# Kernel tuning notes

Measured on AMD Instinct MI355X. Metric: run time of the kernel, lower is better.

## Reference

```python
import jax, jax.numpy as jnp
import numpy as np

B, N, DIM = 4, 8192, 512
HEADS, DIM_HEAD, M, ITERS = 8, 64, 256, 6
KERNEL = 33


def moore_penrose_pinv(x, iters=ITERS):
    # x: [..., m, m]
    abs_x = jnp.abs(x)
    col = abs_x.sum(axis=-1)
    row = abs_x.sum(axis=-2)
    z = jnp.swapaxes(x, -1, -2) / (jnp.max(col) * jnp.max(row))
    I = jnp.eye(x.shape[-1], dtype=x.dtype)
    for _ in range(iters):
        xz = x @ z
        z = 0.25 * z @ (13.0 * I - xz @ (15.0 * I - xz @ (7.0 * I - xz)))
    return z


def setup_inputs() -> dict:
    key = jax.random.key(0)
    k1, k2, k3, k4 = jax.random.split(key, 4)
    x = jax.random.normal(k1, (B, N, DIM), dtype=jnp.float32)
    w_qkv = jax.random.normal(k2, (DIM, 3 * HEADS * DIM_HEAD), dtype=jnp.float32) * 0.02
    w_out = jax.random.normal(k3, (HEADS * DIM_HEAD, DIM), dtype=jnp.float32) * 0.02
    b_out = jnp.zeros((DIM,), dtype=jnp.float32)
    w_conv = jax.random.normal(k4, (HEADS, 1, KERNEL, 1), dtype=jnp.float32) * 0.02
    return {"x": x, "w_qkv": w_qkv, "w_out": w_out, "b_out": b_out, "w_conv": w_conv}


def reference(x, w_qkv, w_out, b_out, w_conv):
    b, n, _ = x.shape
    h, d, m = HEADS, DIM_HEAD, M
    scale = d ** -0.5
    l = n // m  # n is a multiple of m here (padding path is a no-op)

    qkv = x @ w_qkv  # [b, n, 3*h*d]
    q, k, v = jnp.split(qkv, 3, axis=-1)
    to_heads = lambda t: jnp.transpose(t.reshape(b, n, h, d), (0, 2, 1, 3))  # [b,h,n,d]
    q, k, v = to_heads(q), to_heads(k), to_heads(v)

    q = q * scale
    # landmarks: mean over contiguous blocks of length l
    q_land = q.reshape(b, h, m, l, d).sum(axis=3) / l  # [b,h,m,d]
    k_land = k.reshape(b, h, m, l, d).sum(axis=3) / l

    attn1 = jax.nn.softmax(jnp.einsum('bhid,bhjd->bhij', q, k_land), axis=-1)       # [b,h,n,m]
    attn2 = jax.nn.softmax(jnp.einsum('bhid,bhjd->bhij', q_land, k_land), axis=-1)  # [b,h,m,m]
    attn3 = jax.nn.softmax(jnp.einsum('bhid,bhjd->bhij', q_land, k), axis=-1)       # [b,h,m,n]

    attn2_pinv = moore_penrose_pinv(attn2, ITERS)
    out = attn1 @ (attn2_pinv @ (attn3 @ v))  # [b,h,n,d]

    # depthwise residual conv over the sequence axis (kernel (33,1), groups=heads)
    pad = KERNEL // 2
    res = jax.lax.conv_general_dilated(
        v, w_conv, window_strides=(1, 1), padding=((pad, pad), (0, 0)),
        dimension_numbers=('NCHW', 'OIHW', 'NCHW'), feature_group_count=h)
    out = out + res

    out = jnp.transpose(out, (0, 2, 1, 3)).reshape(b, n, h * d)
    out = out @ w_out + b_out
    return out
```

## Files before the change

kernel.cpp:

```cpp
#include <hip/hip_runtime.h>
#include <cstdint>
#include <cstddef>

#define BQ 4
#define NSEQ 8192
#define DIMC 512
#define NH 8
#define DH 64
#define NM 256
#define NITER 6
#define KW 33
#define BHN (BQ*NH)
#define NSLICE 8

typedef unsigned short bf16u;
typedef __attribute__((ext_vector_type(8))) short short8;
typedef __attribute__((ext_vector_type(4))) float f32x4;
#define MFMA16(a,b,c) __builtin_amdgcn_mfma_f32_16x16x32_bf16(a,b,c,0,0,0)

__device__ inline float b2f(bf16u u) { return __uint_as_float(((unsigned int)u) << 16); }
__device__ inline bf16u f2b(float f) {
  unsigned int u = __float_as_uint(f);
  unsigned int r = (u + 0x7fffu + ((u >> 16) & 1u)) >> 16;
  return (bf16u)r;
}
__device__ inline void splt(float v, unsigned short& h, unsigned short& l) {
  unsigned u = __float_as_uint(v);
  h = (unsigned short)(u >> 16);
  float hf = __uint_as_float(u & 0xffff0000u);
  l = (unsigned short)(__float_as_uint(v - hf) >> 16);
}

__global__ __launch_bounds__(256) void k_fill(float* out, int n, float v) {
  int i = blockIdx.x * 256 + threadIdx.x;
  if (i < n) out[i] = v;
}

__global__ __launch_bounds__(256) void c_f2b(const float* __restrict__ src, bf16u* __restrict__ dst, int n8) {
  int i = blockIdx.x*256 + threadIdx.x;
  if (i < n8) {
    const float4* s = (const float4*)(src + (size_t)i*8);
    float4 a = s[0], b = s[1];
    ushort4 lo, hi;
    lo.x=f2b(a.x); lo.y=f2b(a.y); lo.z=f2b(a.z); lo.w=f2b(a.w);
    hi.x=f2b(b.x); hi.y=f2b(b.y); hi.z=f2b(b.z); hi.w=f2b(b.w);
    ushort4* d = (ushort4*)(dst + (size_t)i*8);
    d[0] = lo; d[1] = hi;
  }
}

__global__ __launch_bounds__(256) void c_transb(const float* __restrict__ w, bf16u* __restrict__ wT, int R, int C) {
  int i = blockIdx.x*256 + threadIdx.x;
  if (i < R*C) {
    int r = i / C, c = i - r*C;
    wT[(size_t)c*R + r] = f2b(w[i]);
  }
}

template<int MODE>
__global__ __launch_bounds__(256) void k_mgemm(
    const bf16u* __restrict__ A, const bf16u* __restrict__ Bt, int K, int nb,
    bf16u* __restrict__ oq, bf16u* __restrict__ ok, bf16u* __restrict__ ovT,
    const float* __restrict__ bias, float* __restrict__ oC) {
  __shared__ short As[128][72];
  __shared__ short Bs[128][72];
  const int id = blockIdx.x;
  const int rid = (id & 7) * ((int)gridDim.x >> 3) + (id >> 3);
  const int m0 = (rid / nb) * 128, n0 = (rid % nb) * 128;
  const int t = threadIdx.x;
  const int wid = t>>6, l = t&63, lm = l&15, lg = l>>4;
  const int wr = (wid>>1)*64, wc = (wid&1)*64;
  f32x4 acc[4][4];
  #pragma unroll
  for (int i=0;i<4;++i)
    #pragma unroll
    for (int j=0;j<4;++j) acc[i][j] = (f32x4){0,0,0,0};
  for (int k0=0; k0<K; k0+=64) {
    #pragma unroll
    for (int i=0;i<4;++i) {
      int c = t + i*256;
      int row = c>>3, kc = (c&7)<<3;
      *(uint4*)&As[row][kc] = *(const uint4*)(A  + (size_t)(m0+row)*K + k0+kc);
      *(uint4*)&Bs[row][kc] = *(const uint4*)(Bt + (size_t)(n0+row)*K + k0+kc);
    }
    __syncthreads();
    #pragma unroll
    for (int ks=0;ks<2;++ks) {
      short8 af[4], bfr[4];
      #pragma unroll
      for (int i=0;i<4;++i) {
        af[i]  = *(const short8*)&As[wr+i*16+lm][ks*32+lg*8];
        bfr[i] = *(const short8*)&Bs[wc+i*16+lm][ks*32+lg*8];
      }
      #pragma unroll
      for (int i=0;i<4;++i)
        #pragma unroll
        for (int j=0;j<4;++j)
          acc[i][j] = MFMA16(af[i], bfr[j], acc[i][j]);
    }
    __syncthreads();
  }
  if (MODE==0) {
    #pragma unroll
    for (int mt=0;mt<4;++mt) {
      int grb = m0 + wr + mt*16 + lg*4;
      int b_ = grb>>13, nrow = grb & (NSEQ-1);
      #pragma unroll
      for (int nt=0;nt<4;++nt) {
        int gc = n0 + wc + nt*16 + lm;
        int which = gc>>9, h_ = (gc>>6)&7, d = gc&63;
        if (which==2) {
          ushort4 pk;
          pk.x=f2b(acc[mt][nt][0]); pk.y=f2b(acc[mt][nt][1]);
          pk.z=f2b(acc[mt][nt][2]); pk.w=f2b(acc[mt][nt][3]);
          *(ushort4*)(ovT + (((size_t)b_*NH+h_)*DH + d)*NSEQ + nrow) = pk;
        } else {
          bf16u* dst = (which==0) ? oq : ok;
          float mul = (which==0) ? 0.125f : 1.0f;
          #pragma unroll
          for (int r=0;r<4;++r)
            dst[(((size_t)b_*NH+h_)*NSEQ + nrow + r)*DH + d] = f2b(acc[mt][nt][r]*mul);
        }
      }
    }
  } else {
    #pragma unroll
    for (int mt=0;mt<4;++mt)
      #pragma unroll
      for (int r=0;r<4;++r) {
        int gr = m0 + wr + mt*16 + lg*4 + r;
        #pragma unroll
        for (int nt=0;nt<4;++nt) {
          int gc = n0 + wc + nt*16 + lm;
          oC[(size_t)gr*DIMC + gc] = acc[mt][nt][r] + bias[gc];
        }
      }
  }
}

__global__ __launch_bounds__(256) void k_landmarks(
    const bf16u* __restrict__ q, const bf16u* __restrict__ kbuf,
    float* __restrict__ ql, float* __restrict__ klm,
    bf16u* __restrict__ qlb, bf16u* __restrict__ klmb) {
  int gi = blockIdx.x*4 + (threadIdx.x>>6);
  int d = threadIdx.x & 63;
  int bh = gi >> 8, i = gi & 255;
  size_t srcoff = ((size_t)bh*NSEQ + (size_t)i*32)*DH + d;
  float sq = 0, sk = 0;
  #pragma unroll
  for (int j = 0; j < 32; ++j) {
    sq += b2f(q[srcoff + (size_t)j*DH]);
    sk += b2f(kbuf[srcoff + (size_t)j*DH]);
  }
  float mq = sq * (1.0f/32.0f), mk = sk * (1.0f/32.0f);
  ql[(size_t)gi*DH + d]  = mq;  klm[(size_t)gi*DH + d]  = mk;
  qlb[(size_t)gi*DH + d] = f2b(mq); klmb[(size_t)gi*DH + d] = f2b(mk);
}

__global__ __launch_bounds__(256) void k_qlk_exp(
    const float* __restrict__ A, const float* __restrict__ S, float* __restrict__ C, int K) {
  __shared__ short Ah[128][40], Al[128][40], Bh[64][40], Bl[64][40];
  const int bh = blockIdx.y;
  const size_t abase = (size_t)bh*256*K;
  const size_t cbase = (size_t)bh<<16;
  const int m0 = (blockIdx.x & 1)*128, n0 = (blockIdx.x >> 1)*64;
  const int t = threadIdx.x;
  const int wid = t>>6, l = t&63, lm = l&15, lg = l>>4;
  const int wr = (wid&1)*64, wc = (wid>>1)*32;
  f32x4 acc[4][2];
  #pragma unroll
  for (int i=0;i<4;++i) { acc[i][0] = (f32x4){0,0,0,0}; acc[i][1] = (f32x4){0,0,0,0}; }
  for (int k0=0; k0<K; k0+=32) {
    #pragma unroll
    for (int i=0;i<4;++i) {
      int idx = t + i*256;
      int row = idx>>3, kc = (idx&7)<<2;
      float4 v = *(const float4*)(A + abase + (size_t)(m0+row)*K + k0+kc);
      ushort4 hh, ll;
      splt(v.x, hh.x, ll.x); splt(v.y, hh.y, ll.y);
      splt(v.z, hh.z, ll.z); splt(v.w, hh.w, ll.w);
      *(ushort4*)&Ah[row][kc] = hh; *(ushort4*)&Al[row][kc] = ll;
    }
    #pragma unroll
    for (int i=0;i<2;++i) {
      int idx = t + i*256;
      int row = idx>>3, kc = (idx&7)<<2;
      float4 v = *(const float4*)(S + abase + (size_t)(n0+row)*K + k0+kc);
      ushort4 hh, ll;
      splt(v.x, hh.x, ll.x); splt(v.y, hh.y, ll.y);
      splt(v.z, hh.z, ll.z); splt(v.w, hh.w, ll.w);
      *(ushort4*)&Bh[row][kc] = hh; *(ushort4*)&Bl[row][kc] = ll;
    }
    __syncthreads();
    short8 ah[4], al[4], sh[2], sl[2];
    #pragma unroll
    for (int mt=0;mt<4;++mt) {
      ah[mt] = *(const short8*)&Ah[wr+mt*16+lm][lg*8];
      al[mt] = *(const short8*)&Al[wr+mt*16+lm][lg*8];
    }
    #pragma unroll
    for (int nt=0;nt<2;++nt) {
      sh[nt] = *(const short8*)&Bh[wc+nt*16+lm][lg*8];
      sl[nt] = *(const short8*)&Bl[wc+nt*16+lm][lg*8];
    }
    #pragma unroll
    for (int mt=0;mt<4;++mt)
      #pragma unroll
      for (int nt=0;nt<2;++nt) {
        acc[mt][nt] = MFMA16(ah[mt], sh[nt], acc[mt][nt]);
        acc[mt][nt] = MFMA16(ah[mt], sl[nt], acc[mt][nt]);
        acc[mt][nt] = MFMA16(al[mt], sh[nt], acc[mt][nt]);
      }
    __syncthreads();
  }
  #pragma unroll
  for (int mt=0;mt<4;++mt)
    #pragma unroll
    for (int nt=0;nt<2;++nt)
      #pragma unroll
      for (int r=0;r<4;++r) {
        int gr = m0 + wr + mt*16 + lg*4 + r;
        int gc = n0 + wc + nt*16 + lm;
        C[cbase + (size_t)gr*256 + gc] = __expf(acc[mt][nt][r]);
      }
}

__global__ __launch_bounds__(256) void k_rowsm(float* __restrict__ a2) {
  int row = blockIdx.x*4 + (threadIdx.x>>6);
  int l = threadIdx.x & 63;
  float4* p = (float4*)(a2 + (size_t)row*256 + l*4);
  float4 v = *p;
  float s = v.x+v.y+v.z+v.w;
  #pragma unroll
  for (int d=1; d<64; d<<=1) s += __shfl_xor(s, d);
  float inv = 1.0f/s;
  v.x*=inv; v.y*=inv; v.z*=inv; v.w*=inv;
  *p = v;
}

__global__ void k_zero_scal(unsigned* scal) { if (threadIdx.x < 2) scal[threadIdx.x] = 0u; }

__global__ __launch_bounds__(256) void k_pinv_reduce(const float* __restrict__ a2, unsigned* scal) {
  int bh = blockIdx.x, t = threadIdx.x;
  const float* A = a2 + (size_t)bh*NM*NM;
  float rs = 0, cs = 0;
  for (int j = 0; j < NM; ++j) rs += fabsf(A[(size_t)t*NM + j]);
  for (int i = 0; i < NM; ++i) cs += fabsf(A[(size_t)i*NM + t]);
  __shared__ float red[256];
  red[t] = rs; __syncthreads();
  for (int s = 128; s > 0; s >>= 1) { if (t < s) red[t] = fmaxf(red[t], red[t+s]); __syncthreads(); }
  if (t == 0) atomicMax(scal+0, __float_as_uint(red[0]));
  __syncthreads();
  red[t] = cs; __syncthreads();
  for (int s = 128; s > 0; s >>= 1) { if (t < s) red[t] = fmaxf(red[t], red[t+s]); __syncthreads(); }
  if (t == 0) atomicMax(scal+1, __float_as_uint(red[0]));
}

__global__ __launch_bounds__(256) void k_split_init(
    const float* __restrict__ a2, const unsigned* __restrict__ scal,
    bf16u* __restrict__ a2h, bf16u* __restrict__ a2l,
    bf16u* __restrict__ zch, bf16u* __restrict__ zcl) {
  __shared__ bf16u Th[64][72], Tl[64][72];
  const int bh = blockIdx.y;
  const int tx = blockIdx.x & 3, ty = blockIdx.x >> 2;
  const int r0 = ty*64, c0 = tx*64;
  const size_t base = (size_t)bh<<16;
  const int t = threadIdx.x;
  const float rc = 1.0f/(__uint_as_float(scal[0]) * __uint_as_float(scal[1]));
  {
    int rr = t>>2, cc0 = (t&3)*16;
    const float* src = a2 + base + (size_t)(r0+rr)*256 + c0+cc0;
    bf16u hbuf[16], lbuf[16];
    #pragma unroll
    for (int u=0;u<4;++u) {
      float4 v = *(const float4*)(src + u*4);
      float vv[4] = {v.x,v.y,v.z,v.w};
      #pragma unroll
      for (int e=0;e<4;++e) {
        splt(vv[e], hbuf[u*4+e], lbuf[u*4+e]);
        bf16u zh_, zl_;
        splt(vv[e]*rc, zh_, zl_);
        Th[cc0+u*4+e][rr] = zh_;
        Tl[cc0+u*4+e][rr] = zl_;
      }
    }
    bf16u* dh = a2h + base + (size_t)(r0+rr)*256 + c0+cc0;
    bf16u* dl = a2l + base + (size_t)(r0+rr)*256 + c0+cc0;
    #pragma unroll
    for (int u=0;u<4;++u) {
      *(ushort4*)(dh + u*4) = *(ushort4*)&hbuf[u*4];
      *(ushort4*)(dl + u*4) = *(ushort4*)&lbuf[u*4];
    }
  }
  __syncthreads();
  {
    int cc = t>>2, rr0 = (t&3)*16;
    bf16u* dh = zch + base + (size_t)(c0+cc)*256 + r0+rr0;
    bf16u* dl = zcl + base + (size_t)(c0+cc)*256 + r0+rr0;
    #pragma unroll
    for (int u=0;u<4;++u) {
      *(ushort4*)(dh + u*4) = *(ushort4*)&Th[cc][rr0+u*4];
      *(ushort4*)(dl + u*4) = *(ushort4*)&Tl[cc][rr0+u*4];
    }
  }
}

template<int PHASE>
__global__ __launch_bounds__(256) void k_ns(
    const bf16u* __restrict__ Ah, const bf16u* __restrict__ Al,
    const bf16u* __restrict__ A2h, const bf16u* __restrict__ A2l,
    const bf16u* __restrict__ Bh_, const bf16u* __restrict__ Bl_,
    const bf16u* __restrict__ Xh, const bf16u* __restrict__ Xl,
    const bf16u* __restrict__ X2h, const bf16u* __restrict__ X2l,
    bf16u* __restrict__ Oh, bf16u* __restrict__ Ol,
    bf16u* __restrict__ O2h, bf16u* __restrict__ O2l,
    bf16u* __restrict__ Ch, bf16u* __restrict__ Cl,
    const unsigned* __restrict__ scal) {
  __shared__ short AhS[128][36], AlS[128][36], BhS[64][36], BlS[64][36];
  const int z = (gridDim.z == 2) ? blockIdx.z : (PHASE==2 ? 1 : 0);
  const int bh = blockIdx.y;
  const size_t base = (size_t)bh<<16;
  const int m0 = (blockIdx.x & 1)*128, n0 = (blockIdx.x >> 1)*64;
  const int t = threadIdx.x;
  const int wid = t>>6, l = t&63, lm = l&15, lg = l>>4;
  const int wr = (wid&1)*64, wc = (wid>>1)*32;
  const bf16u* pAh = z ? A2h : Ah;
  const bf16u* pAl = z ? A2l : Al;
  f32x4 acc[4][2];
  #pragma unroll
  for (int i=0;i<4;++i) { acc[i][0] = (f32x4){0,0,0,0}; acc[i][1] = (f32x4){0,0,0,0}; }
  for (int k0=0; k0<256; k0+=32) {
    #pragma unroll
    for (int i=0;i<2;++i) {
      int idx = t + i*256;
      int row = idx>>2, ch = (idx&3)<<3;
      *(uint4*)&AhS[row][ch] = *(const uint4*)(pAh + base + (size_t)(m0+row)*256 + k0+ch);
      *(uint4*)&AlS[row][ch] = *(const uint4*)(pAl + base + (size_t)(m0+row)*256 + k0+ch);
    }
    {
      int row = t>>2, ch = (t&3)<<3;
      *(uint4*)&BhS[row][ch] = *(const uint4*)(Bh_ + base + (size_t)(n0+row)*256 + k0+ch);
      *(uint4*)&BlS[row][ch] = *(const uint4*)(Bl_ + base + (size_t)(n0+row)*256 + k0+ch);
    }
    __syncthreads();
    short8 ah[4], al[4], sh[2], sl[2];
    #pragma unroll
    for (int mt=0;mt<4;++mt) {
      ah[mt] = *(const short8*)&AhS[wr+mt*16+lm][lg*8];
      al[mt] = *(const short8*)&AlS[wr+mt*16+lm][lg*8];
    }
    #pragma unroll
    for (int nt=0;nt<2;++nt) {
      sh[nt] = *(const short8*)&BhS[wc+nt*16+lm][lg*8];
      sl[nt] = *(const short8*)&BlS[wc+nt*16+lm][lg*8];
    }
    #pragma unroll
    for (int mt=0;mt<4;++mt)
      #pragma unroll
      for (int nt=0;nt<2;++nt) {
        acc[mt][nt] = MFMA16(ah[mt], sh[nt], acc[mt][nt]);
        acc[mt][nt] = MFMA16(ah[mt], sl[nt], acc[mt][nt]);
        acc[mt][nt] = MFMA16(al[mt], sh[nt], acc[mt][nt]);
      }
    __syncthreads();
  }
  float rc = 1.0f;
  if (PHASE==0) rc = 1.0f/(__uint_as_float(scal[0]) * __uint_as_float(scal[1]));
  #pragma unroll
  for (int mt=0;mt<4;++mt)
    #pragma unroll
    for (int nt=0;nt<2;++nt)
      #pragma unroll
      for (int r=0;r<4;++r) {
        int gr = m0 + wr + mt*16 + lg*4 + r;
        int gc = n0 + wc + nt*16 + lm;
        size_t idx = base + (size_t)gr*256 + gc;
        float a = acc[mt][nt][r];
        bf16u hh, ll;
        if (PHASE==0) {
          splt(a*rc, hh, ll); Oh[idx]=hh; Ol[idx]=ll;
        } else if (PHASE==1) {
          if (z==0) {
            splt(a, hh, ll); Oh[idx]=hh; Ol[idx]=ll;
            float wv = b2f(Xh[idx]) + b2f(Xl[idx]);
            float cb = ((gr==gc)?15.0f:0.0f) - 7.0f*wv + a;
            splt(cb, hh, ll); Ch[idx]=hh; Cl[idx]=ll;
          } else {
            splt(a, hh, ll); O2h[idx]=hh; O2l[idx]=ll;
          }
        } else {
          if (z==0) {
            float xv = b2f(Xh[idx]) + b2f(Xl[idx]);
            splt(3.25f*xv - 0.25f*a, hh, ll); Oh[idx]=hh; Ol[idx]=ll;
          } else {
            float xv = b2f(X2h[idx]) + b2f(X2l[idx]);
            splt(3.25f*xv - 0.25f*a, hh, ll); O2h[idx]=hh; O2l[idx]=ll;
          }
        }
      }
}

template<int MODE>
__global__ __launch_bounds__(256) void k_flash(
    const bf16u* __restrict__ qg, const bf16u* __restrict__ kg,
    const bf16u* __restrict__ vtg, float* __restrict__ fpart, bf16u* __restrict__ outb) {
  constexpr int NCH = (MODE==0) ? 16 : 4;
  const int bh = blockIdx.y;
  const int tile = blockIdx.x;
  const int t = threadIdx.x;
  const int wid = t>>6, l = t&63, lm = l&15, lg = l>>4;
  const size_t NQbase = (MODE==0) ? ((size_t)bh*NM) : ((size_t)bh*NSEQ + (size_t)tile*256);
  const int NJ = (MODE==0) ? NSEQ : NM;
  const int j0base = (MODE==0) ? tile*1024 : 0;

  __shared__ short Ks[64][72];
  __shared__ short Vs[64][72];
  __shared__ short Pt[4][64][72];

  short8 qf[4][2];
  {
    const bf16u* qrow = qg + (NQbase + (size_t)wid*64) * DH;
    #pragma unroll
    for (int mt=0;mt<4;++mt)
      #pragma unroll
      for (int ks=0;ks<2;++ks)
        qf[mt][ks] = *(const short8*)(qrow + (size_t)(mt*16+lm)*DH + ks*32 + lg*8);
  }
  f32x4 oacc[4][4];
  #pragma unroll
  for (int i=0;i<4;++i)
    #pragma unroll
    for (int j=0;j<4;++j) oacc[i][j] = (f32x4){0,0,0,0};
  float rs[4][4];
  #pragma unroll
  for (int i=0;i<4;++i) { rs[i][0]=0; rs[i][1]=0; rs[i][2]=0; rs[i][3]=0; }

  const bf16u* kbh = kg  + (size_t)bh*NJ*DH;
  const bf16u* vbh = vtg + (size_t)bh*DH*NJ;

  for (int ch=0; ch<NCH; ++ch) {
    int j0 = j0base + ch*64;
    #pragma unroll
    for (int i=0;i<2;++i) {
      int c = t + i*256;
      int row = c>>3, kc = (c&7)<<3;
      *(uint4*)&Ks[row][kc] = *(const uint4*)(kbh + (size_t)(j0+row)*DH + kc);
      *(uint4*)&Vs[row][kc] = *(const uint4*)(vbh + (size_t)row*NJ + j0 + kc);
    }
    __syncthreads();
    short8 kf[4][2];
    #pragma unroll
    for (int jt=0;jt<4;++jt)
      #pragma unroll
      for (int ks=0;ks<2;++ks)
        kf[jt][ks] = *(const short8*)&Ks[jt*16+lm][ks*32+lg*8];
    #pragma unroll
    for (int mt=0;mt<4;++mt) {
      #pragma unroll
      for (int jt=0;jt<4;++jt) {
        f32x4 s = (f32x4){0,0,0,0};
        s = MFMA16(qf[mt][0], kf[jt][0], s);
        s = MFMA16(qf[mt][1], kf[jt][1], s);
        #pragma unroll
        for (int r=0;r<4;++r) {
          float p = __expf(s[r]);
          rs[mt][r] += p;
          Pt[wid][mt*16+lg*4+r][jt*16+lm] = f2b(p);
        }
      }
    }
    short8 vf[4][2];
    #pragma unroll
    for (int dt=0;dt<4;++dt)
      #pragma unroll
      for (int jw=0;jw<2;++jw)
        vf[dt][jw] = *(const short8*)&Vs[dt*16+lm][jw*32+lg*8];
    #pragma unroll
    for (int mt=0;mt<4;++mt) {
      short8 pa0 = *(const short8*)&Pt[wid][mt*16+lm][lg*8];
      short8 pa1 = *(const short8*)&Pt[wid][mt*16+lm][32+lg*8];
      #pragma unroll
      for (int dt=0;dt<4;++dt) {
        oacc[mt][dt] = MFMA16(pa0, vf[dt][0], oacc[mt][dt]);
        oacc[mt][dt] = MFMA16(pa1, vf[dt][1], oacc[mt][dt]);
      }
    }
    __syncthreads();
  }
  #pragma unroll
  for (int mt=0;mt<4;++mt)
    #pragma unroll
    for (int r=0;r<4;++r) {
      float v = rs[mt][r];
      v += __shfl_xor(v, 1); v += __shfl_xor(v, 2);
      v += __shfl_xor(v, 4); v += __shfl_xor(v, 8);
      rs[mt][r] = v;
    }
  if (MODE==0) {
    float* fb = fpart + (((size_t)bh*NSLICE + tile)*NM)*65;
    #pragma unroll
    for (int mt=0;mt<4;++mt)
      #pragma unroll
      for (int r=0;r<4;++r) {
        int row = wid*64 + mt*16 + lg*4 + r;
        float* fr = fb + (size_t)row*65;
        #pragma unroll
        for (int dt=0;dt<4;++dt) fr[dt*16+lm] = oacc[mt][dt][r];
        if (lm==0) fr[64] = rs[mt][r];
      }
  } else {
    const int b_ = bh>>3, h_ = bh&7;
    #pragma unroll
    for (int mt=0;mt<4;++mt)
      #pragma unroll
      for (int r=0;r<4;++r) {
        float inv = 1.0f/rs[mt][r];
        int n = tile*256 + wid*64 + mt*16 + lg*4 + r;
        bf16u* orow = outb + ((size_t)b_*NSEQ + n)*DIMC + h_*DH;
        #pragma unroll
        for (int dt=0;dt<4;++dt)
          orow[dt*16+lm] = f2b(oacc[mt][dt][r]*inv);
      }
  }
}

__global__ __launch_bounds__(256) void k_attn3v_combine(
    const float* __restrict__ fpart, float* __restrict__ w1T) {
  int gi = blockIdx.x*4 + (threadIdx.x>>6);
  int d = threadIdx.x & 63;
  int bh = gi >> 8, i = gi & 255;
  float accd = 0, ssum = 0;
  #pragma unroll
  for (int s = 0; s < NSLICE; ++s) {
    const float* fp = fpart + (((size_t)bh*NSLICE + s)*NM + i)*65;
    accd += fp[d];
    ssum += fp[64];
  }
  w1T[((size_t)bh*64 + d)*256 + i] = accd / ssum;
}

__global__ __launch_bounds__(256) void k_w2nat(
    const float* __restrict__ w1T, const bf16u* __restrict__ zh, const bf16u* __restrict__ zl,
    bf16u* __restrict__ w2T) {
  __shared__ short Ah[64][36], Al[64][36], Bh[64][36], Bl[64][36];
  const int bh = blockIdx.y;
  const int n0 = blockIdx.x*64;
  const size_t a0 = (size_t)bh*64*256;
  const size_t s0 = (size_t)bh<<16;
  const int t = threadIdx.x;
  const int wid = t>>6, l = t&63, lm = l&15, lg = l>>4;
  const int wc = wid*16;
  f32x4 acc[4];
  #pragma unroll
  for (int i=0;i<4;++i) acc[i] = (f32x4){0,0,0,0};
  for (int k0=0; k0<256; k0+=32) {
    #pragma unroll
    for (int i=0;i<2;++i) {
      int idx = t + i*256;
      int row = idx>>3, kc = (idx&7)<<2;
      float4 v = *(const float4*)(w1T + a0 + (size_t)row*256 + k0+kc);
      ushort4 hh, ll;
      splt(v.x, hh.x, ll.x); splt(v.y, hh.y, ll.y);
      splt(v.z, hh.z, ll.z); splt(v.w, hh.w, ll.w);
      *(ushort4*)&Ah[row][kc] = hh; *(ushort4*)&Al[row][kc] = ll;
    }
    {
      int row = t>>2, ch = (t&3)<<3;
      *(uint4*)&Bh[row][ch] = *(const uint4*)(zh + s0 + (size_t)(n0+row)*256 + k0+ch);
      *(uint4*)&Bl[row][ch] = *(const uint4*)(zl + s0 + (size_t)(n0+row)*256 + k0+ch);
    }
    __syncthreads();
    short8 sh = *(const short8*)&Bh[wc+lm][lg*8];
    short8 sl = *(const short8*)&Bl[wc+lm][lg*8];
    #pragma unroll
    for (int mt=0;mt<4;++mt) {
      short8 ah = *(const short8*)&Ah[mt*16+lm][lg*8];
      short8 al = *(const short8*)&Al[mt*16+lm][lg*8];
      acc[mt] = MFMA16(ah, sh, acc[mt]);
      acc[mt] = MFMA16(ah, sl, acc[mt]);
      acc[mt] = MFMA16(al, sh, acc[mt]);
    }
    __syncthreads();
  }
  #pragma unroll
  for (int mt=0;mt<4;++mt)
    #pragma unroll
    for (int r=0;r<4;++r) {
      int gm = mt*16 + lg*4 + r;
      w2T[a0 + (size_t)gm*256 + n0 + wc + lm] = f2b(acc[mt][r]);
    }
}

__global__ __launch_bounds__(256) void k_conv_add(
    const bf16u* __restrict__ vt, const float* __restrict__ wc, bf16u* __restrict__ outb) {
  __shared__ short Vs[288][72];
  __shared__ float Wsh[40];
  const int bh = blockIdx.y, n0 = blockIdx.x*256;
  const int b_ = bh>>3, h_ = bh&7;
  const int t = threadIdx.x;
  if (t < KW) Wsh[t] = wc[h_*KW + t];
  const bf16u* vrow = vt + (size_t)bh*DH*NSEQ;
  {
    int d = t&63, seg = t>>6;
    #pragma unroll
    for (int u=0; u<9; ++u) {
      int nl = seg*72 + u*8;
      int gn = n0 - 16 + nl;
      bf16u e8[8];
      if (gn >= 0 && gn + 8 <= NSEQ) {
        *(uint4*)e8 = *(const uint4*)(vrow + (size_t)d*NSEQ + gn);
      } else {
        #pragma unroll
        for (int e=0;e<8;++e) {
          int g = gn + e;
          e8[e] = (g>=0 && g<NSEQ) ? vrow[(size_t)d*NSEQ + g] : (bf16u)0;
        }
      }
      #pragma unroll
      for (int e=0;e<8;++e) Vs[nl+e][d] = e8[e];
    }
  }
  __syncthreads();
  const int d = t&63, q = t>>6;
  #pragma unroll
  for (int c2=0;c2<4;++c2) {
    int nb = q*64 + c2*16;
    float wv[48];
    #pragma unroll
    for (int i=0;i<48;++i) wv[i] = b2f(Vs[nb+i][d]);
    #pragma unroll
    for (int e=0;e<16;++e) {
      float s = 0;
      #pragma unroll
      for (int k=0;k<KW;++k) s = fmaf(wv[e+k], Wsh[k], s);
      size_t oi = ((size_t)b_*NSEQ + n0 + nb + e)*DIMC + h_*DH + d;
      outb[oi] = f2b(b2f(outb[oi]) + s);
    }
  }
}

extern "C" void kernel_launch(void* const* d_in, const int* in_sizes, int n_in,
                              void* d_out, int out_size, void* d_ws, size_t ws_size,
                              hipStream_t stream) {
  (void)in_sizes; (void)n_in;
  const float* x      = (const float*)d_in[0];
  const float* w_qkv  = (const float*)d_in[1];
  const float* w_out  = (const float*)d_in[2];
  const float* b_out  = (const float*)d_in[3];
  const float* w_conv = (const float*)d_in[4];
  float* out = (float*)d_out;

  const size_t QKV_E = (size_t)BHN*NSEQ*DH;
  const size_t LM_E  = (size_t)BHN*NM*DH;
  const size_t MM_E  = (size_t)BHN*NM*NM;
  const size_t PLSZ  = MM_E*2;

  char* p = (char*)d_ws;
  char* nsb   = p;          p += 10*PLSZ;
  bf16u* qb    = (bf16u*)p; p += QKV_E*2;
  bf16u* kb    = (bf16u*)p; p += QKV_E*2;
  bf16u* vT    = (bf16u*)p; p += QKV_E*2;
  bf16u* wqkvT = (bf16u*)p; p += (size_t)DIMC*3*DIMC*2;
  bf16u* woutT = (bf16u*)p; p += (size_t)DIMC*DIMC*2;
  float* ql    = (float*)p; p += LM_E*4;
  float* klm   = (float*)p; p += LM_E*4;
  bf16u* qlb   = (bf16u*)p; p += LM_E*2;
  bf16u* klmb  = (bf16u*)p; p += LM_E*2;
  float* w1T   = (float*)p; p += LM_E*4;
  bf16u* w2T   = (bf16u*)p; p += LM_E*2;
  unsigned* scal = (unsigned*)p; p += 256;
  size_t need = (size_t)(p - (char*)d_ws);

  if (ws_size < need) {
    k_fill<<<(out_size + 255)/256, 256, 0, stream>>>(out, out_size, 12345.0f);
    return;
  }

  bf16u* a2h  = (bf16u*)(nsb + 0*PLSZ);
  bf16u* a2l  = (bf16u*)(nsb + 1*PLSZ);
  bf16u* s1h  = (bf16u*)(nsb + 2*PLSZ);
  bf16u* s1l  = (bf16u*)(nsb + 3*PLSZ);
  bf16u* cmh  = (bf16u*)(nsb + 4*PLSZ);
  bf16u* cml  = (bf16u*)(nsb + 5*PLSZ);
  bf16u* wh   = (bf16u*)(nsb + 6*PLSZ);
  bf16u* wl   = (bf16u*)(nsb + 7*PLSZ);
  bf16u* zch  = (bf16u*)(nsb + 8*PLSZ);
  bf16u* zcl  = (bf16u*)(nsb + 9*PLSZ);
  float* a2f  = (float*)(nsb + 2*PLSZ);
  float* fpart = (float*)nsb;
  bf16u* c1h = a2h; bf16u* c1l = a2l;
  bf16u* xb  = qb;
  xb = (bf16u*)nsb;

  c_f2b<<<(int)(QKV_E/8/256), 256, 0, stream>>>(x, xb, (int)(QKV_E/8));
  c_transb<<<(DIMC*3*DIMC+255)/256, 256, 0, stream>>>(w_qkv, wqkvT, DIMC, 3*DIMC);
  c_transb<<<(DIMC*DIMC+255)/256, 256, 0, stream>>>(w_out, woutT, DIMC, DIMC);
  k_mgemm<0><<<3072, 256, 0, stream>>>(xb, wqkvT, DIMC, 12, qb, kb, vT, nullptr, nullptr);
  k_landmarks<<<(BHN*NM)/4, 256, 0, stream>>>(qb, kb, ql, klm, qlb, klmb);
  k_qlk_exp<<<dim3(8, BHN), 256, 0, stream>>>(ql, klm, a2f, DH);
  k_rowsm<<<BHN*NM/4, 256, 0, stream>>>(a2f);
  k_zero_scal<<<1, 64, 0, stream>>>(scal);
  k_pinv_reduce<<<BHN, 256, 0, stream>>>(a2f, scal);
  k_split_init<<<dim3(16, BHN), 256, 0, stream>>>(a2f, scal, a2h, a2l, zch, zcl);
  k_ns<0><<<dim3(8, BHN, 1), 256, 0, stream>>>(
      a2h,a2l, nullptr,nullptr, a2h,a2l, nullptr,nullptr, nullptr,nullptr,
      wh,wl, nullptr,nullptr, nullptr,nullptr, scal);
  for (int it = 0; it < NITER; ++it) {
    k_ns<1><<<dim3(8, BHN, 2), 256, 0, stream>>>(
        wh,wl, zch,zcl, wh,wl, wh,wl, nullptr,nullptr,
        s1h,s1l, c1h,c1l, cmh,cml, nullptr);
    k_ns<2><<<dim3(8, BHN, (it==NITER-1)?1:2), 256, 0, stream>>>(
        s1h,s1l, c1h,c1l, cmh,cml, wh,wl, zch,zcl,
        wh,wl, zch,zcl, nullptr,nullptr, nullptr);
  }
  k_flash<0><<<dim3(NSLICE, BHN), 256, 0, stream>>>(qlb, kb, vT, fpart, nullptr);
  k_attn3v_combine<<<(BHN*NM)/4, 256, 0, stream>>>(fpart, w1T);
  k_w2nat<<<dim3(4, BHN), 256, 0, stream>>>(w1T, zch, zcl, w2T);
  bf16u* outb = kb;
  k_flash<1><<<dim3(NSEQ/256, BHN), 256, 0, stream>>>(qb, klmb, w2T, nullptr, outb);
  k_conv_add<<<dim3(NSEQ/256, BHN), 256, 0, stream>>>(vT, w_conv, outb);
  k_mgemm<1><<<1024, 256, 0, stream>>>(outb, woutT, DIMC, 4, nullptr, nullptr, nullptr, b_out, out);
}
```

Before: 712.3 us.

## Merge prep conversion kernels, fold scalar zeroing, and double flash split slices

```diff
diff --git a/kernel.cpp b/kernel.cpp
--- a/kernel.cpp
+++ b/kernel.cpp
@@ -11,7 +11,8 @@
 #define NITER 6
 #define KW 33
 #define BHN (BQ*NH)
-#define NSLICE 8
+#define NSLICE 16
+#define JS (NSEQ/NSLICE)
 
 typedef unsigned short bf16u;
 typedef __attribute__((ext_vector_type(8))) short short8;
@@ -36,24 +37,27 @@
   if (i < n) out[i] = v;
 }
 
-__global__ __launch_bounds__(256) void c_f2b(const float* __restrict__ src, bf16u* __restrict__ dst, int n8) {
-  int i = blockIdx.x*256 + threadIdx.x;
-  if (i < n8) {
-    const float4* s = (const float4*)(src + (size_t)i*8);
+__global__ __launch_bounds__(256) void c_prep(
+    const float* __restrict__ x, const float* __restrict__ w_qkv, const float* __restrict__ w_out,
+    bf16u* __restrict__ xb, bf16u* __restrict__ wqkvT, bf16u* __restrict__ woutT) {
+  int id = blockIdx.x;
+  if (id < 8192) {
+    int i = id*256 + threadIdx.x;
+    const float4* s = (const float4*)(x + (size_t)i*8);
     float4 a = s[0], b = s[1];
     ushort4 lo, hi;
     lo.x=f2b(a.x); lo.y=f2b(a.y); lo.z=f2b(a.z); lo.w=f2b(a.w);
     hi.x=f2b(b.x); hi.y=f2b(b.y); hi.z=f2b(b.z); hi.w=f2b(b.w);
-    ushort4* d = (ushort4*)(dst + (size_t)i*8);
+    ushort4* d = (ushort4*)(xb + (size_t)i*8);
     d[0] = lo; d[1] = hi;
-  }
-}
-
-__global__ __launch_bounds__(256) void c_transb(const float* __restrict__ w, bf16u* __restrict__ wT, int R, int C) {
-  int i = blockIdx.x*256 + threadIdx.x;
-  if (i < R*C) {
-    int r = i / C, c = i - r*C;
-    wT[(size_t)c*R + r] = f2b(w[i]);
+  } else if (id < 8192+3072) {
+    int i = (id-8192)*256 + threadIdx.x;
+    int r = i / 1536, c = i - r*1536;
+    wqkvT[(size_t)c*DIMC + r] = f2b(w_qkv[i]);
+  } else {
+    int i = (id-11264)*256 + threadIdx.x;
+    int r = i >> 9, c = i & 511;
+    woutT[(size_t)c*DIMC + r] = f2b(w_out[i]);
   }
 }
 
@@ -225,7 +229,8 @@
       }
 }
 
-__global__ __launch_bounds__(256) void k_rowsm(float* __restrict__ a2) {
+__global__ __launch_bounds__(256) void k_rowsm(float* __restrict__ a2, unsigned* __restrict__ scal) {
+  if (blockIdx.x == 0 && threadIdx.x < 2) scal[threadIdx.x] = 0u;
   int row = blockIdx.x*4 + (threadIdx.x>>6);
   int l = threadIdx.x & 63;
   float4* p = (float4*)(a2 + (size_t)row*256 + l*4);
@@ -237,8 +242,6 @@
   v.x*=inv; v.y*=inv; v.z*=inv; v.w*=inv;
   *p = v;
 }
-
-__global__ void k_zero_scal(unsigned* scal) { if (threadIdx.x < 2) scal[threadIdx.x] = 0u; }
 
 __global__ __launch_bounds__(256) void k_pinv_reduce(const float* __restrict__ a2, unsigned* scal) {
   int bh = blockIdx.x, t = threadIdx.x;
@@ -404,14 +407,14 @@
 __global__ __launch_bounds__(256) void k_flash(
     const bf16u* __restrict__ qg, const bf16u* __restrict__ kg,
     const bf16u* __restrict__ vtg, float* __restrict__ fpart, bf16u* __restrict__ outb) {
-  constexpr int NCH = (MODE==0) ? 16 : 4;
+  constexpr int NCH = (MODE==0) ? (JS/64) : 4;
   const int bh = blockIdx.y;
   const int tile = blockIdx.x;
   const int t = threadIdx.x;
   const int wid = t>>6, l = t&63, lm = l&15, lg = l>>4;
   const size_t NQbase = (MODE==0) ? ((size_t)bh*NM) : ((size_t)bh*NSEQ + (size_t)tile*256);
   const int NJ = (MODE==0) ? NSEQ : NM;
-  const int j0base = (MODE==0) ? tile*1024 : 0;
+  const int j0base = (MODE==0) ? tile*JS : 0;
 
   __shared__ short Ks[64][72];
   __shared__ short Vs[64][72];
@@ -656,7 +659,9 @@
   const size_t PLSZ  = MM_E*2;
 
   char* p = (char*)d_ws;
-  char* nsb   = p;          p += 10*PLSZ;
+  char* nsb   = p;          p += 9*PLSZ;
+  bf16u* zch  = (bf16u*)p;  p += PLSZ;
+  bf16u* zcl  = (bf16u*)p;  p += PLSZ;
   bf16u* qb    = (bf16u*)p; p += QKV_E*2;
   bf16u* kb    = (bf16u*)p; p += QKV_E*2;
   bf16u* vT    = (bf16u*)p; p += QKV_E*2;
@@ -684,22 +689,16 @@
   bf16u* cml  = (bf16u*)(nsb + 5*PLSZ);
   bf16u* wh   = (bf16u*)(nsb + 6*PLSZ);
   bf16u* wl   = (bf16u*)(nsb + 7*PLSZ);
-  bf16u* zch  = (bf16u*)(nsb + 8*PLSZ);
-  bf16u* zcl  = (bf16u*)(nsb + 9*PLSZ);
   float* a2f  = (float*)(nsb + 2*PLSZ);
   float* fpart = (float*)nsb;
   bf16u* c1h = a2h; bf16u* c1l = a2l;
-  bf16u* xb  = qb;
-  xb = (bf16u*)nsb;
-
-  c_f2b<<<(int)(QKV_E/8/256), 256, 0, stream>>>(x, xb, (int)(QKV_E/8));
-  c_transb<<<(DIMC*3*DIMC+255)/256, 256, 0, stream>>>(w_qkv, wqkvT, DIMC, 3*DIMC);
-  c_transb<<<(DIMC*DIMC+255)/256, 256, 0, stream>>>(w_out, woutT, DIMC, DIMC);
+  bf16u* xb  = (bf16u*)nsb;
+
+  c_prep<<<12288, 256, 0, stream>>>(x, w_qkv, w_out, xb, wqkvT, woutT);
   k_mgemm<0><<<3072, 256, 0, stream>>>(xb, wqkvT, DIMC, 12, qb, kb, vT, nullptr, nullptr);
   k_landmarks<<<(BHN*NM)/4, 256, 0, stream>>>(qb, kb, ql, klm, qlb, klmb);
   k_qlk_exp<<<dim3(8, BHN), 256, 0, stream>>>(ql, klm, a2f, DH);
-  k_rowsm<<<BHN*NM/4, 256, 0, stream>>>(a2f);
-  k_zero_scal<<<1, 64, 0, stream>>>(scal);
+  k_rowsm<<<BHN*NM/4, 256, 0, stream>>>(a2f, scal);
   k_pinv_reduce<<<BHN, 256, 0, stream>>>(a2f, scal);
   k_split_init<<<dim3(16, BHN), 256, 0, stream>>>(a2f, scal, a2h, a2l, zch, zcl);
   k_ns<0><<<dim3(8, BHN, 1), 256, 0, stream>>>(
```

Result: faster. 688.2 us (-3.4%).
